# Kernel tuning notes

Measured on AMD Instinct MI355X. Metric: run time of the kernel, lower is better.

Reference implementation:

```python
import jax, jax.numpy as jnp
import numpy as np

B, L, D, H = 32, 1024, 512, 512
ODE_STEPS = 6
DT = 1.0

def _unif(key, shape, fan_in):
    bound = 1.0 / np.sqrt(fan_in)
    return jax.random.uniform(key, shape, jnp.float32, -bound, bound)

def setup_inputs() -> dict:
    key = jax.random.key(0)
    ks = jax.random.split(key, 9)
    return {
        "x": jax.random.normal(ks[0], (B, L, D), jnp.float32),
        "log_tau": jnp.zeros((H,), jnp.float32),
        "W_in": _unif(ks[1], (H, D), D),
        "b_in": _unif(ks[2], (H,), D),
        "W_rec": _unif(ks[3], (H, H), H),
        "W_gate": _unif(ks[4], (H, D + H), D + H),
        "b_gate": _unif(ks[5], (H,), D + H),
        "W_out": _unif(ks[6], (H, H), H),
        "b_out": _unif(ks[7], (H,), H),
    }

def reference(x, log_tau, W_in, b_in, W_rec, W_gate, b_gate, W_out, b_out):
    Bx, Lx, Dx = x.shape
    Hx = log_tau.shape[0]
    tau = jnp.exp(log_tau)                      # (H,)
    sub_dt = DT / ODE_STEPS
    # Split gate weight: cat([x, h]) @ W_gate.T == x @ Wg_x.T + h @ Wg_h.T
    Wg_x, Wg_h = W_gate[:, :Dx], W_gate[:, Dx:]
    # Precompute input-dependent drives for the whole sequence (time-parallel GEMMs)
    drive = jnp.einsum('bld,hd->blh', x, W_in) + b_in      # W_in(x), (B,L,H)
    gate_x = jnp.einsum('bld,hd->blh', x, Wg_x) + b_gate   # input part of gate pre-act

    def step(h, inp):
        d, gx = inp  # (B,H) each
        for _ in range(ODE_STEPS):  # small fixed unroll of ODE sub-steps
            rec = h @ W_rec.T
            gate = jax.nn.sigmoid(gx + h @ Wg_h.T)
            f = -h + gate * jnp.tanh(d + rec)
            h = h + (sub_dt / tau) * f
        return h, h

    h0 = jnp.zeros((Bx, Hx), x.dtype)
    h_last, fwd = jax.lax.scan(step, h0, (drive.transpose(1, 0, 2), gate_x.transpose(1, 0, 2)))
    fwd = fwd.transpose(1, 0, 2)                 # (B,L,H)
    output = fwd @ W_out.T + b_out               # output_proj; dropout is identity (p=0)
    return output, h_last
```

## Files before the change

### kernel.cpp

```cpp
#include <hip/hip_runtime.h>

typedef unsigned short u16;
typedef unsigned int   u32;
typedef unsigned long long u64;

#define LTC_B 32
#define LTC_L 1024
#define LTC_D 512
#define LTC_H 512
#define NG 8
#define NP 16
#define NBG 4

typedef _Float16 f16x8  __attribute__((ext_vector_type(8)));
typedef _Float16 f16x2t __attribute__((ext_vector_type(2)));
typedef float    f32x4  __attribute__((ext_vector_type(4)));

static __device__ __forceinline__ u32 packh(float a, float b) {
    f16x2t p; p[0] = (_Float16)a; p[1] = (_Float16)b;
    return __builtin_bit_cast(u32, p);
}
static __device__ __forceinline__ float unplo(u32 w) {
    return (float)__builtin_bit_cast(f16x2t, w)[0];
}
static __device__ __forceinline__ float unphi(u32 w) {
    return (float)__builtin_bit_cast(f16x2t, w)[1];
}
static __device__ __forceinline__ float sigm(float x) {
    return 1.f / (1.f + __expf(-x));
}
static __device__ __forceinline__ float tanh_f(float x) {
    float e = __expf(2.f * x);
    return 1.f - 2.f / (e + 1.f);
}
static __device__ __forceinline__ f16x8 cvt8(const float* p) {
    const float4 a = *(const float4*)p;
    const float4 b = *(const float4*)(p + 4);
    f16x8 r;
    r[0] = (_Float16)a.x; r[1] = (_Float16)a.y; r[2] = (_Float16)a.z; r[3] = (_Float16)a.w;
    r[4] = (_Float16)b.x; r[5] = (_Float16)b.y; r[6] = (_Float16)b.z; r[7] = (_Float16)b.w;
    return r;
}
static __device__ __forceinline__ bool stamp4(u64 a, u64 b, u64 c, u64 d, u32 k) {
    return ((u32)(a >> 32) == k) & ((u32)(b >> 32) == k) &
           ((u32)(c >> 32) == k) & ((u32)(d >> 32) == k);
}

__global__ __launch_bounds__(256) void gemm_a32_c16(
    const float* __restrict__ A, const float* __restrict__ W, int ldb,
    const float* __restrict__ bias, u16* __restrict__ C)
{
    const int wave = threadIdx.x >> 6;
    const int lane = threadIdx.x & 63;
    const int tile = blockIdx.x * 4 + wave;
    const int nt = tile & 7;
    const int mt = tile >> 3;
    const int r16 = lane & 15;
    const int kq  = (lane >> 4) * 8;

    const float* ap = A + (size_t)(mt * 64 + r16) * LTC_D + kq;
    const float* wp = W + (size_t)(nt * 64 + r16) * ldb + kq;

    f32x4 acc[4][4];
    #pragma unroll
    for (int i = 0; i < 4; ++i)
        #pragma unroll
        for (int jj = 0; jj < 4; ++jj) acc[i][jj] = (f32x4){0.f, 0.f, 0.f, 0.f};

    for (int ks = 0; ks < 16; ++ks) {
        f16x8 af[4], bf[4];
        #pragma unroll
        for (int t = 0; t < 4; ++t) {
            af[t] = cvt8(ap + (size_t)t * 16 * LTC_D + ks * 32);
            bf[t] = cvt8(wp + (size_t)t * 16 * ldb  + ks * 32);
        }
        #pragma unroll
        for (int mi = 0; mi < 4; ++mi)
            #pragma unroll
            for (int ni = 0; ni < 4; ++ni)
                acc[mi][ni] = __builtin_amdgcn_mfma_f32_16x16x32_f16(
                    af[mi], bf[ni], acc[mi][ni], 0, 0, 0);
    }
    const int row = (lane >> 4) * 4;
    const int col = lane & 15;
    #pragma unroll
    for (int ni = 0; ni < 4; ++ni) {
        const int n = nt * 64 + ni * 16 + col;
        const float bv = bias[n];
        #pragma unroll
        for (int mi = 0; mi < 4; ++mi)
            #pragma unroll
            for (int r = 0; r < 4; ++r) {
                _Float16 h = (_Float16)(acc[mi][ni][r] + bv);
                C[(size_t)(mt * 64 + mi * 16 + row + r) * LTC_H + n] =
                    __builtin_bit_cast(u16, h);
            }
    }
}

__global__ __launch_bounds__(256) void gemm_a16_c32(
    const u16* __restrict__ A, const float* __restrict__ W,
    const float* __restrict__ bias, float* __restrict__ C)
{
    const int wave = threadIdx.x >> 6;
    const int lane = threadIdx.x & 63;
    const int tile = blockIdx.x * 4 + wave;
    const int nt = tile & 7;
    const int mt = tile >> 3;
    const int r16 = lane & 15;
    const int kq  = (lane >> 4) * 8;

    const _Float16* ap = (const _Float16*)A + (size_t)(mt * 64 + r16) * LTC_D + kq;
    const float*    wp = W + (size_t)(nt * 64 + r16) * LTC_H + kq;

    f32x4 acc[4][4];
    #pragma unroll
    for (int i = 0; i < 4; ++i)
        #pragma unroll
        for (int jj = 0; jj < 4; ++jj) acc[i][jj] = (f32x4){0.f, 0.f, 0.f, 0.f};

    for (int ks = 0; ks < 16; ++ks) {
        f16x8 af[4], bf[4];
        #pragma unroll
        for (int t = 0; t < 4; ++t) {
            af[t] = *(const f16x8*)(ap + (size_t)t * 16 * LTC_D + ks * 32);
            bf[t] = cvt8(wp + (size_t)t * 16 * LTC_H + ks * 32);
        }
        #pragma unroll
        for (int mi = 0; mi < 4; ++mi)
            #pragma unroll
            for (int ni = 0; ni < 4; ++ni)
                acc[mi][ni] = __builtin_amdgcn_mfma_f32_16x16x32_f16(
                    af[mi], bf[ni], acc[mi][ni], 0, 0, 0);
    }
    const int row = (lane >> 4) * 4;
    const int col = lane & 15;
    #pragma unroll
    for (int ni = 0; ni < 4; ++ni) {
        const int n = nt * 64 + ni * 16 + col;
        const float bv = bias[n];
        #pragma unroll
        for (int mi = 0; mi < 4; ++mi)
            #pragma unroll
            for (int r = 0; r < 4; ++r)
                C[(size_t)(mt * 64 + mi * 16 + row + r) * LTC_H + n] =
                    acc[mi][ni][r] + bv;
    }
}

__global__ __launch_bounds__(256) void ltc_scan(
    u32* __restrict__ drive,
    const u32* __restrict__ gatex,
    const float* __restrict__ W_rec,
    const float* __restrict__ W_gate,
    const float* __restrict__ log_tau,
    u64* __restrict__ hbuf,
    float* __restrict__ hlast)
{
    const int g   = blockIdx.x & 7;
    const int p   = blockIdx.x >> 3;
    const int tid = threadIdx.x;
    const int lane = tid & 63;
    const int wv   = tid >> 6;

    __shared__ u32 hTu[16][260];
    __shared__ float red[64][17];

    const int nl = wv * 16 + (lane & 15);
    const int kq = (lane >> 4) * 8;
    const float* wrow = (nl < 32)
        ? (W_rec  + (size_t)(32 * p + nl) * LTC_H)
        : (W_gate + (size_t)(32 * p + nl - 32) * (LTC_D + LTC_H) + LTC_D);
    f16x8 Wf[16];
    #pragma unroll
    for (int ks = 0; ks < 16; ++ks) Wf[ks] = cvt8(wrow + ks * 32 + kq);

    for (int i = tid; i < 16 * 260; i += 256) (&hTu[0][0])[i] = 0;
    __syncthreads();

    const int ub = tid >> 4;
    const int jp = tid & 15;
    const int j0 = 32 * p + 2 * jp;
    const int gb = g * NBG + ub;
    float h0 = 0.f, h1 = 0.f, stau0 = 0.f, stau1 = 0.f;
    size_t dwofs = 0;
    if (tid < 64) {
        stau0 = (1.f / 6.f) * __expf(-log_tau[j0]);
        stau1 = (1.f / 6.f) * __expf(-log_tau[j0 + 1]);
        dwofs = (size_t)gb * LTC_L * 256 + 16 * p + jp;
    }

    const _Float16* hrow = (const _Float16*)&hTu[lane & 15][0];
    u32 kp1 = 0;
    int budget = 1 << 22;

    u32 dw = 0, gw = 0;
    if (tid < 64) { dw = drive[dwofs]; gw = gatex[dwofs]; }

    for (int l = 0; l < LTC_L; ++l) {
        const float d0 = unplo(dw), d1 = unphi(dw);
        const float gx0 = unplo(gw), gx1 = unphi(gw);
        u32 dn = 0, gn = 0;
        if (tid < 64 && l + 1 < LTC_L) {
            dn = drive[dwofs + (size_t)(l + 1) * 256];
            gn = gatex[dwofs + (size_t)(l + 1) * 256];
        }
        #pragma unroll 1
        for (int s = 0; s < 6; ++s) {
            f32x4 acc0 = (f32x4){0.f, 0.f, 0.f, 0.f}, acc1 = acc0;
            #pragma unroll
            for (int ks = 0; ks < 16; ks += 2) {
                const f16x8 a0 = *(const f16x8*)(hrow + ks * 32 + kq);
                const f16x8 a1 = *(const f16x8*)(hrow + (ks + 1) * 32 + kq);
                acc0 = __builtin_amdgcn_mfma_f32_16x16x32_f16(a0, Wf[ks],     acc0, 0, 0, 0);
                acc1 = __builtin_amdgcn_mfma_f32_16x16x32_f16(a1, Wf[ks + 1], acc1, 0, 0, 0);
            }
            {
                const int n  = wv * 16 + (lane & 15);
                const int rb = (lane >> 4) * 4;
                #pragma unroll
                for (int r = 0; r < 4; ++r) red[n][rb + r] = acc0[r] + acc1[r];
            }
            __syncthreads();
            ++kp1;
            const size_t pbase = (size_t)((kp1 & 1u) * NG + g) * (NBG * 256);
            if (tid < 64) {
                const float rec0 = red[2 * jp][ub],     gh0 = red[32 + 2 * jp][ub];
                const float rec1 = red[2 * jp + 1][ub], gh1 = red[32 + 2 * jp + 1][ub];
                h0 += stau0 * (sigm(gx0 + gh0) * tanh_f(d0 + rec0) - h0);
                h1 += stau1 * (sigm(gx1 + gh1) * tanh_f(d1 + rec1) - h1);
                const u64 v = ((u64)kp1 << 32) | (u64)packh(h0, h1);
                __hip_atomic_store(hbuf + pbase + (size_t)ub * 256 + 16 * p + jp,
                                   v, __ATOMIC_RELAXED, __HIP_MEMORY_SCOPE_AGENT);
            }
            {
                const u64* sb = hbuf + pbase + tid;
                u64 a0, a1, a2, a3;
                bool ok;
                do {
                    a0 = __hip_atomic_load(sb,       __ATOMIC_RELAXED,
                                           __HIP_MEMORY_SCOPE_AGENT);
                    a1 = __hip_atomic_load(sb + 256, __ATOMIC_RELAXED,
                                           __HIP_MEMORY_SCOPE_AGENT);
                    a2 = __hip_atomic_load(sb + 512, __ATOMIC_RELAXED,
                                           __HIP_MEMORY_SCOPE_AGENT);
                    a3 = __hip_atomic_load(sb + 768, __ATOMIC_RELAXED,
                                           __HIP_MEMORY_SCOPE_AGENT);
                    ok = stamp4(a0, a1, a2, a3, kp1);
                } while (!ok && --budget > 0);
                hTu[0][tid] = (u32)a0; hTu[1][tid] = (u32)a1;
                hTu[2][tid] = (u32)a2; hTu[3][tid] = (u32)a3;
            }
            __syncthreads();
        }
        if (tid < 64) drive[dwofs + (size_t)l * 256] = packh(h0, h1);
        dw = dn; gw = gn;
    }
    if (tid < 64) {
        hlast[(size_t)gb * LTC_H + j0]     = h0;
        hlast[(size_t)gb * LTC_H + j0 + 1] = h1;
    }
}

extern "C" void kernel_launch(void* const* d_in, const int* in_sizes, int n_in,
                              void* d_out, int out_size, void* d_ws, size_t ws_size,
                              hipStream_t stream)
{
    const float* x       = (const float*)d_in[0];
    const float* log_tau = (const float*)d_in[1];
    const float* W_in    = (const float*)d_in[2];
    const float* b_in    = (const float*)d_in[3];
    const float* W_rec   = (const float*)d_in[4];
    const float* W_gate  = (const float*)d_in[5];
    const float* b_gate  = (const float*)d_in[6];
    const float* W_out   = (const float*)d_in[7];
    const float* b_out   = (const float*)d_in[8];

    float* out   = (float*)d_out;
    float* hlast = out + (size_t)LTC_B * LTC_L * LTC_H;

    u32* ws    = (u32*)d_ws;
    u32* drive = ws;
    u32* gatex = ws + 8388608;
    u64* hbuf  = (u64*)(ws + 16777216);

    const int blocks = (LTC_B * LTC_L / 64) * (LTC_H / 64) / 4;

    gemm_a32_c16<<<blocks, 256, 0, stream>>>(x, W_in, LTC_D, b_in, (u16*)drive);
    gemm_a32_c16<<<blocks, 256, 0, stream>>>(x, W_gate, LTC_D + LTC_H, b_gate, (u16*)gatex);
    ltc_scan<<<NG * NP, 256, 0, stream>>>(drive, gatex, W_rec, W_gate, log_tau,
                                          hbuf, hlast);
    gemm_a16_c32<<<blocks, 256, 0, stream>>>((const u16*)drive, W_out, b_out, out);
}
```

Before: 10.81 ms.

## Halve scan partitions, keep both weight halves per wave, drop the reduction barrier

```diff
diff --git a/kernel.cpp b/kernel.cpp
--- a/kernel.cpp
+++ b/kernel.cpp
@@ -9,7 +9,7 @@
 #define LTC_D 512
 #define LTC_H 512
 #define NG 8
-#define NP 16
+#define NP 8
 #define NBG 4
 
 typedef _Float16 f16x8  __attribute__((ext_vector_type(8)));
@@ -148,7 +148,7 @@
     }
 }
 
-__global__ __launch_bounds__(256) void ltc_scan(
+__global__ __launch_bounds__(256, 1) void ltc_scan(
     u32* __restrict__ drive,
     const u32* __restrict__ gatex,
     const float* __restrict__ W_rec,
@@ -163,75 +163,104 @@
     const int lane = tid & 63;
     const int wv   = tid >> 6;
 
-    __shared__ u32 hTu[16][260];
-    __shared__ float red[64][17];
-
-    const int nl = wv * 16 + (lane & 15);
-    const int kq = (lane >> 4) * 8;
-    const float* wrow = (nl < 32)
-        ? (W_rec  + (size_t)(32 * p + nl) * LTC_H)
-        : (W_gate + (size_t)(32 * p + nl - 32) * (LTC_D + LTC_H) + LTC_D);
-    f16x8 Wf[16];
-    #pragma unroll
-    for (int ks = 0; ks < 16; ++ks) Wf[ks] = cvt8(wrow + ks * 32 + kq);
-
-    for (int i = tid; i < 16 * 260; i += 256) (&hTu[0][0])[i] = 0;
+    __shared__ u32 hTu[2][16][260];
+
+    const int rowb = 64 * p + 16 * wv;
+    const int brow = rowb + (lane & 15);
+    const int kq   = (lane >> 4) * 8;
+
+    f16x8 WfR[16], WfG[16];
+    {
+        const float* wr = W_rec  + (size_t)brow * LTC_H + kq;
+        const float* wg = W_gate + (size_t)brow * (LTC_D + LTC_H) + LTC_D + kq;
+        #pragma unroll
+        for (int ks = 0; ks < 16; ++ks) {
+            WfR[ks] = cvt8(wr + ks * 32);
+            WfG[ks] = cvt8(wg + ks * 32);
+        }
+    }
+
+    for (int i = tid; i < 2 * 16 * 260; i += 256) (&hTu[0][0][0])[i] = 0;
+
+    const int n = rowb + lane;
+    const int hodd = lane & 1;
+    float h[4] = {0.f, 0.f, 0.f, 0.f};
+    float stau = 0.f;
+    size_t dofs[4] = {0, 0, 0, 0};
+    u32 dw[4] = {0, 0, 0, 0}, gw[4] = {0, 0, 0, 0};
+    if (lane < 16) {
+        stau = (1.f / 6.f) * __expf(-log_tau[n]);
+        #pragma unroll
+        for (int r = 0; r < 4; ++r)
+            dofs[r] = (size_t)(g * NBG + r) * LTC_L * 256 + (n >> 1);
+        #pragma unroll
+        for (int r = 0; r < 4; ++r) { dw[r] = drive[dofs[r]]; gw[r] = gatex[dofs[r]]; }
+    }
     __syncthreads();
 
-    const int ub = tid >> 4;
-    const int jp = tid & 15;
-    const int j0 = 32 * p + 2 * jp;
-    const int gb = g * NBG + ub;
-    float h0 = 0.f, h1 = 0.f, stau0 = 0.f, stau1 = 0.f;
-    size_t dwofs = 0;
-    if (tid < 64) {
-        stau0 = (1.f / 6.f) * __expf(-log_tau[j0]);
-        stau1 = (1.f / 6.f) * __expf(-log_tau[j0 + 1]);
-        dwofs = (size_t)gb * LTC_L * 256 + 16 * p + jp;
-    }
-
-    const _Float16* hrow = (const _Float16*)&hTu[lane & 15][0];
+    const u32* hbase = &hTu[0][lane & 15][(lane >> 4) * 4];
     u32 kp1 = 0;
     int budget = 1 << 22;
 
-    u32 dw = 0, gw = 0;
-    if (tid < 64) { dw = drive[dwofs]; gw = gatex[dwofs]; }
-
     for (int l = 0; l < LTC_L; ++l) {
-        const float d0 = unplo(dw), d1 = unphi(dw);
-        const float gx0 = unplo(gw), gx1 = unphi(gw);
-        u32 dn = 0, gn = 0;
-        if (tid < 64 && l + 1 < LTC_L) {
-            dn = drive[dwofs + (size_t)(l + 1) * 256];
-            gn = gatex[dwofs + (size_t)(l + 1) * 256];
-        }
+        float d_[4], gx_[4];
+        if (lane < 16) {
+            #pragma unroll
+            for (int r = 0; r < 4; ++r) {
+                d_[r]  = hodd ? unphi(dw[r]) : unplo(dw[r]);
+                gx_[r] = hodd ? unphi(gw[r]) : unplo(gw[r]);
+            }
+        }
+        u32 dn_[4] = {0, 0, 0, 0}, gn_[4] = {0, 0, 0, 0};
+        if (lane < 16 && l + 1 < LTC_L) {
+            #pragma unroll
+            for (int r = 0; r < 4; ++r) {
+                dn_[r] = drive[dofs[r] + (size_t)(l + 1) * 256];
+                gn_[r] = gatex[dofs[r] + (size_t)(l + 1) * 256];
+            }
+        }
+        u32 pw[4] = {0, 0, 0, 0};
         #pragma unroll 1
         for (int s = 0; s < 6; ++s) {
-            f32x4 acc0 = (f32x4){0.f, 0.f, 0.f, 0.f}, acc1 = acc0;
+            const u32* hb = hbase + (kp1 & 1u) * (16 * 260);
+            f32x4 aR0 = (f32x4){0.f, 0.f, 0.f, 0.f};
+            f32x4 aR1 = aR0, aG0 = aR0, aG1 = aR0;
             #pragma unroll
             for (int ks = 0; ks < 16; ks += 2) {
-                const f16x8 a0 = *(const f16x8*)(hrow + ks * 32 + kq);
-                const f16x8 a1 = *(const f16x8*)(hrow + (ks + 1) * 32 + kq);
-                acc0 = __builtin_amdgcn_mfma_f32_16x16x32_f16(a0, Wf[ks],     acc0, 0, 0, 0);
-                acc1 = __builtin_amdgcn_mfma_f32_16x16x32_f16(a1, Wf[ks + 1], acc1, 0, 0, 0);
-            }
-            {
-                const int n  = wv * 16 + (lane & 15);
-                const int rb = (lane >> 4) * 4;
-                #pragma unroll
-                for (int r = 0; r < 4; ++r) red[n][rb + r] = acc0[r] + acc1[r];
-            }
-            __syncthreads();
+                const f16x8 a0 = *(const f16x8*)(hb + ks * 16);
+                const f16x8 a1 = *(const f16x8*)(hb + ks * 16 + 16);
+                aR0 = __builtin_amdgcn_mfma_f32_16x16x32_f16(a0, WfR[ks],     aR0, 0, 0, 0);
+                aG0 = __builtin_amdgcn_mfma_f32_16x16x32_f16(a0, WfG[ks],     aG0, 0, 0, 0);
+                aR1 = __builtin_amdgcn_mfma_f32_16x16x32_f16(a1, WfR[ks + 1], aR1, 0, 0, 0);
+                aG1 = __builtin_amdgcn_mfma_f32_16x16x32_f16(a1, WfG[ks + 1], aG1, 0, 0, 0);
+            }
             ++kp1;
             const size_t pbase = (size_t)((kp1 & 1u) * NG + g) * (NBG * 256);
-            if (tid < 64) {
-                const float rec0 = red[2 * jp][ub],     gh0 = red[32 + 2 * jp][ub];
-                const float rec1 = red[2 * jp + 1][ub], gh1 = red[32 + 2 * jp + 1][ub];
-                h0 += stau0 * (sigm(gx0 + gh0) * tanh_f(d0 + rec0) - h0);
-                h1 += stau1 * (sigm(gx1 + gh1) * tanh_f(d1 + rec1) - h1);
-                const u64 v = ((u64)kp1 << 32) | (u64)packh(h0, h1);
-                __hip_atomic_store(hbuf + pbase + (size_t)ub * 256 + 16 * p + jp,
-                                   v, __ATOMIC_RELAXED, __HIP_MEMORY_SCOPE_AGENT);
+            if (lane < 16) {
+                #pragma unroll
+                for (int r = 0; r < 4; ++r) {
+                    const float rec = aR0[r] + aR1[r];
+                    const float gh  = aG0[r] + aG1[r];
+                    h[r] += stau * (sigm(gx_[r] + gh) * tanh_f(d_[r] + rec) - h[r]);
+                }
+                const float e0 = __shfl_xor(h[0], 1);
+                const float e1 = __shfl_xor(h[1], 1);
+                const float e2 = __shfl_xor(h[2], 1);
+                const float e3 = __shfl_xor(h[3], 1);
+                if (!hodd) {
+                    pw[0] = packh(h[0], e0); pw[1] = packh(h[1], e1);
+                    pw[2] = packh(h[2], e2); pw[3] = packh(h[3], e3);
+                    const u64 st = (u64)kp1 << 32;
+                    u64* pb = hbuf + pbase + (n >> 1);
+                    __hip_atomic_store(pb,       st | pw[0], __ATOMIC_RELAXED,
+                                       __HIP_MEMORY_SCOPE_AGENT);
+                    __hip_atomic_store(pb + 256, st | pw[1], __ATOMIC_RELAXED,
+                                       __HIP_MEMORY_SCOPE_AGENT);
+                    __hip_atomic_store(pb + 512, st | pw[2], __ATOMIC_RELAXED,
+                                       __HIP_MEMORY_SCOPE_AGENT);
+                    __hip_atomic_store(pb + 768, st | pw[3], __ATOMIC_RELAXED,
+                                       __HIP_MEMORY_SCOPE_AGENT);
+                }
             }
             {
                 const u64* sb = hbuf + pbase + tid;
@@ -248,17 +277,26 @@
                                            __HIP_MEMORY_SCOPE_AGENT);
                     ok = stamp4(a0, a1, a2, a3, kp1);
                 } while (!ok && --budget > 0);
-                hTu[0][tid] = (u32)a0; hTu[1][tid] = (u32)a1;
-                hTu[2][tid] = (u32)a2; hTu[3][tid] = (u32)a3;
+                u32* ht = &hTu[kp1 & 1u][0][0];
+                ht[tid]       = (u32)a0;
+                ht[260 + tid] = (u32)a1;
+                ht[520 + tid] = (u32)a2;
+                ht[780 + tid] = (u32)a3;
             }
             __syncthreads();
         }
-        if (tid < 64) drive[dwofs + (size_t)l * 256] = packh(h0, h1);
-        dw = dn; gw = gn;
-    }
-    if (tid < 64) {
-        hlast[(size_t)gb * LTC_H + j0]     = h0;
-        hlast[(size_t)gb * LTC_H + j0 + 1] = h1;
+        if (lane < 16 && !hodd) {
+            #pragma unroll
+            for (int r = 0; r < 4; ++r)
+                drive[dofs[r] + (size_t)l * 256] = pw[r];
+        }
+        #pragma unroll
+        for (int r = 0; r < 4; ++r) { dw[r] = dn_[r]; gw[r] = gn_[r]; }
+    }
+    if (lane < 16) {
+        #pragma unroll
+        for (int r = 0; r < 4; ++r)
+            hlast[(size_t)(g * NBG + r) * LTC_H + n] = h[r];
     }
 }
 
```

After: 13.46 ms. 24.5% more time.
